# Performance work log

Measured on AMD Instinct MI355X. Metric: run time of the kernel, lower is better.

Reference implementation:

```python
import jax, jax.numpy as jnp
import numpy as np

B, NBLK, D, DY, NDIM, NMC, DH = 4096, 12, 2, 2, 24, 256, 100
SQRT3 = 3.0 ** 0.5
G2 = np.array([[1.0, 0.0], [0.5, SQRT3 / 2.0]], dtype=np.float32)
G = jnp.asarray(np.kron(np.eye(NBLK, dtype=np.float32), G2))  # (24,24) block-diag hexagonal generator
LOG_VOL = (NDIM // 2) * float(np.log(SQRT3 / 2.0))  # log sqrt(det(G G^T))


def _lin(x, w, b=None):
    y = x @ w.T
    return y if b is None else y + b


def _hex_quantize(y):
    # Exact nearest-point quantizer for the product-of-A2 (hexagonal) lattice.
    p = y.reshape(y.shape[:-1] + (NDIM // 2, 2))
    off = jnp.array([0.5, SQRT3 / 2.0], dtype=y.dtype)
    def rnd(q):  # round to rectangular sublattice Z x sqrt(3)Z
        return jnp.stack([jnp.round(q[..., 0]), jnp.round(q[..., 1] / SQRT3) * SQRT3], axis=-1)
    c0 = rnd(p)
    c1 = rnd(p - off) + off
    d0 = jnp.sum((p - c0) ** 2, axis=-1)
    d1 = jnp.sum((p - c1) ** 2, axis=-1)
    return jnp.where((d0 <= d1)[..., None], c0, c1).reshape(y.shape)


def _logits_cumulative(v, Hs, bs, fs):
    # compressai-style per-channel monotone cumulative network. v: (..., C) -> (..., C)
    v = v[..., None]  # (..., C, 1)
    for k in range(len(Hs)):
        v = jnp.einsum('coi,...ci->...co', jax.nn.softplus(Hs[k]), v) + bs[k][:, :, 0]
        if k < len(fs):
            v = v + jnp.tanh(fs[k][:, :, 0]) * jnp.tanh(v)
    return v[..., 0]


def setup_inputs() -> dict:
    key = jax.random.key(0)
    ks = iter(jax.random.split(key, 64))
    def nrm(shape, s=1.0):
        return jax.random.normal(next(ks), shape, jnp.float32) * s
    inp = {}
    inp['x'] = nrm((B, NBLK, D))
    inp['y_mean'] = nrm((NBLK, DY))
    inp['u'] = jax.random.uniform(next(ks), (NMC, NDIM), jnp.float32)
    inp['ga_w0'] = nrm((DH, D), D ** -0.5); inp['ga_b0'] = jnp.zeros((DH,), jnp.float32)
    inp['ga_w1'] = nrm((DH, DH), DH ** -0.5); inp['ga_b1'] = jnp.zeros((DH,), jnp.float32)
    inp['ga_w2'] = nrm((DY, DH), DH ** -0.5); inp['ga_b2'] = jnp.zeros((DY,), jnp.float32)
    inp['gs_w0'] = nrm((DH, DY), DY ** -0.5); inp['gs_b0'] = jnp.zeros((DH,), jnp.float32)
    inp['gs_w1'] = nrm((DH, DH), DH ** -0.5); inp['gs_b1'] = jnp.zeros((DH,), jnp.float32)
    inp['gs_w2'] = nrm((D, DH), DH ** -0.5); inp['gs_b2'] = jnp.zeros((D,), jnp.float32)
    inp['gac_w0'] = nrm((DH, NDIM), NDIM ** -0.5)
    inp['gac_w1'] = nrm((DH, DH), DH ** -0.5)
    inp['gac_w2'] = nrm((NDIM, DH), DH ** -0.5)
    inp['gsc_w0'] = nrm((DH, NDIM), NDIM ** -0.5)
    inp['gsc_w1'] = nrm((DH, DH), DH ** -0.5)
    inp['gsc_w2'] = nrm((NDIM, DH), DH ** -0.5)
    # factorized-prior cumulative params, layer dims 1->3->3->3->3->1
    inp['eb_H0'] = nrm((NDIM, 3, 1), 0.5)
    inp['eb_H1'] = nrm((NDIM, 3, 3), 0.5)
    inp['eb_H2'] = nrm((NDIM, 3, 3), 0.5)
    inp['eb_H3'] = nrm((NDIM, 3, 3), 0.5)
    inp['eb_H4'] = nrm((NDIM, 1, 3), 0.5)
    inp['eb_b0'] = nrm((NDIM, 3, 1), 0.5)
    inp['eb_b1'] = nrm((NDIM, 3, 1), 0.5)
    inp['eb_b2'] = nrm((NDIM, 3, 1), 0.5)
    inp['eb_b3'] = nrm((NDIM, 3, 1), 0.5)
    inp['eb_b4'] = nrm((NDIM, 1, 1), 0.5)
    inp['eb_a0'] = nrm((NDIM, 3, 1), 0.5)
    inp['eb_a1'] = nrm((NDIM, 3, 1), 0.5)
    inp['eb_a2'] = nrm((NDIM, 3, 1), 0.5)
    inp['eb_a3'] = nrm((NDIM, 3, 1), 0.5)
    return inp


def reference(x, y_mean, u, ga_w0, ga_b0, ga_w1, ga_b1, ga_w2, ga_b2,
              gs_w0, gs_b0, gs_w1, gs_b1, gs_w2, gs_b2,
              gac_w0, gac_w1, gac_w2, gsc_w0, gsc_w1, gsc_w2,
              eb_H0, eb_H1, eb_H2, eb_H3, eb_H4,
              eb_b0, eb_b1, eb_b2, eb_b3, eb_b4,
              eb_a0, eb_a1, eb_a2, eb_a3):
    lrelu, sp = jax.nn.leaky_relu, jax.nn.softplus
    # analysis transform g_a: (B, 12, 2) -> (B, 12, dy)
    y1 = _lin(lrelu(_lin(lrelu(_lin(x, ga_w0, ga_b0)), ga_w1, ga_b1)), ga_w2, ga_b2)
    # EMA zero-mean update (buffer assignment => no gradient through the mean)
    ym = jax.lax.stop_gradient(0.05 * y_mean + 0.95 * jnp.mean(y1, axis=0))
    y1 = (y1 - ym).reshape(B, NDIM)
    # coupled analysis transform g_a_c (Softplus MLP, no bias)
    y1 = _lin(sp(_lin(sp(_lin(y1, gac_w0)), gac_w1)), gac_w2)
    # quasi-uniform samples from the Voronoi cell of the lattice origin
    u2 = u @ G
    u2 = u2 - _hex_quantize(u2)
    # lattice quantization with straight-through estimator
    y_q = _hex_quantize(y1)
    y_hat = y1 + jax.lax.stop_gradient(y_q - y1)
    # Monte-Carlo log-likelihood over the Voronoi cell with factorized prior density
    Hs = (eb_H0, eb_H1, eb_H2, eb_H3, eb_H4)
    bs = (eb_b0, eb_b1, eb_b2, eb_b3, eb_b4)
    fs = (eb_a0, eb_a1, eb_a2, eb_a3)
    pts = y_hat[:, None, :] + u2[None, :, :]  # (B, NMC, NDIM)
    def cdf(p):
        return jax.nn.sigmoid(_logits_cumulative(p, Hs, bs, fs))
    _, pdf = jax.jvp(cdf, (pts,), (jnp.ones_like(pts),))  # density = d/dx cdf(x)
    logp = jnp.sum(jnp.log(pdf + 1e-9), axis=-1)  # (B, NMC)
    lik = jax.scipy.special.logsumexp(logp, axis=1) - jnp.log(jnp.float32(NMC)) + LOG_VOL  # (B,)
    # synthesis transforms
    y_hat1 = _lin(sp(_lin(sp(_lin(y_hat, gsc_w0)), gsc_w1)), gsc_w2).reshape(B, NBLK, DY) + ym
    x_hat = _lin(lrelu(_lin(lrelu(_lin(y_hat1, gs_w0, gs_b0)), gs_w1, gs_b1)), gs_w2, gs_b2)
    return (x_hat, lik)
```

## Files before the change

### kernel.cpp

```cpp
#include <hip/hip_runtime.h>
#include <hip/hip_bf16.h>
#include <math.h>
#include <limits.h>

constexpr int NB    = 4096;
constexpr int ROWS2 = NB * 12;
constexpr int GA_BLOCKS = ROWS2 / 128;
constexpr int GS_BLOCKS = ROWS2 / 64;
constexpr int TBL_CAP = 64;
constexpr int KBASE   = -32;

constexpr size_t WS_Y1    = 0;
constexpr size_t WS_YHAT  = 98304;
constexpr size_t WS_YHAT1 = 196608;
constexpr size_t WS_YM    = 294912;
constexpr size_t WS_U2T   = 294936;
constexpr size_t WS_EB    = 301080;
constexpr size_t WS_PART  = 302472;
constexpr size_t WS_W1T   = 320904;
constexpr size_t WS_W1BF  = 359304;
constexpr size_t WS_TBL   = 366472;
constexpr size_t WS_END   = WS_TBL + 24 * TBL_CAP * 256;

constexpr float STEP_ODD = 0.8660254037844386f;
constexpr float INV_ODD  = 1.1547005383792517f;

typedef __attribute__((ext_vector_type(8))) short bf16x8;
typedef __attribute__((ext_vector_type(4))) float f32x4;

__device__ __forceinline__ float lrelu(float x) { return x >= 0.f ? x : 0.01f * x; }
__device__ __forceinline__ float rcp_fast(float x) { return __builtin_amdgcn_rcpf(x); }

__device__ __forceinline__ unsigned short f2bf(float f) {
    unsigned b = __float_as_uint(f);
    b += 0x7FFFu + ((b >> 16) & 1u);
    return (unsigned short)(b >> 16);
}

__device__ __forceinline__ float tanh_fast(float x) {
    float xx = fminf(fmaxf(x, -15.f), 15.f);
    float e = __expf(xx + xx);
    return fmaf(-2.f, rcp_fast(e + 1.f), 1.f);
}
__device__ __forceinline__ float splus(float x) {
    return fmaxf(x, 0.f) + __logf(1.f + __expf(-fabsf(x)));
}
__device__ __forceinline__ float splus_precise(float x) {
    return fmaxf(x, 0.f) + log1pf(expf(-fabsf(x)));
}

__device__ __forceinline__ void fma4(float4& a, float h, const float4& w) {
    a.x = fmaf(h, w.x, a.x); a.y = fmaf(h, w.y, a.y);
    a.z = fmaf(h, w.z, a.z); a.w = fmaf(h, w.w, a.w);
}

__device__ __forceinline__ void hexq(float p0, float p1, float& q0, float& q1) {
    const float S3 = 1.7320508075688772f;
    const float H3 = 0.8660254037844386f;
    float c00 = rintf(p0);
    float c01 = rintf(p1 / S3) * S3;
    float c10 = rintf(p0 - 0.5f) + 0.5f;
    float c11 = rintf((p1 - H3) / S3) * S3 + H3;
    float d0 = (p0 - c00) * (p0 - c00) + (p1 - c01) * (p1 - c01);
    float d1 = (p0 - c10) * (p0 - c10) + (p1 - c11) * (p1 - c11);
    bool take0 = d0 <= d1;
    q0 = take0 ? c00 : c10;
    q1 = take0 ? c01 : c11;
}

__device__ __forceinline__ float logpdf_ch(const float* __restrict__ P, float p) {
    float w00 = P[0], w01 = P[1], w02 = P[2];
    float z0 = fmaf(w00, p, P[3]);
    float z1 = fmaf(w01, p, P[4]);
    float z2 = fmaf(w02, p, P[5]);
    float a0 = P[6], a1 = P[7], a2 = P[8];
    float e0 = tanh_fast(z0), e1 = tanh_fast(z1), e2 = tanh_fast(z2);
    float h0 = fmaf(a0, e0, z0), h1 = fmaf(a1, e1, z1), h2 = fmaf(a2, e2, z2);
    float t0 = w00 * fmaf(a0, fmaf(-e0, e0, 1.f), 1.f);
    float t1 = w01 * fmaf(a1, fmaf(-e1, e1, 1.f), 1.f);
    float t2 = w02 * fmaf(a2, fmaf(-e2, e2, 1.f), 1.f);

#define EB_LAYER(O)                                                            \
    {                                                                          \
        float z0n = fmaf(P[O+0], h0, fmaf(P[O+1], h1, fmaf(P[O+2], h2, P[O+9])));  \
        float z1n = fmaf(P[O+3], h0, fmaf(P[O+4], h1, fmaf(P[O+5], h2, P[O+10]))); \
        float z2n = fmaf(P[O+6], h0, fmaf(P[O+7], h1, fmaf(P[O+8], h2, P[O+11]))); \
        float s0 = fmaf(P[O+0], t0, fmaf(P[O+1], t1, P[O+2] * t2));            \
        float s1 = fmaf(P[O+3], t0, fmaf(P[O+4], t1, P[O+5] * t2));            \
        float s2 = fmaf(P[O+6], t0, fmaf(P[O+7], t1, P[O+8] * t2));            \
        float g0 = P[O+12], g1 = P[O+13], g2 = P[O+14];                        \
        float q0 = tanh_fast(z0n), q1 = tanh_fast(z1n), q2 = tanh_fast(z2n);   \
        h0 = fmaf(g0, q0, z0n); h1 = fmaf(g1, q1, z1n); h2 = fmaf(g2, q2, z2n); \
        t0 = s0 * fmaf(g0, fmaf(-q0, q0, 1.f), 1.f);                           \
        t1 = s1 * fmaf(g1, fmaf(-q1, q1, 1.f), 1.f);                           \
        t2 = s2 * fmaf(g2, fmaf(-q2, q2, 1.f), 1.f);                           \
    }
    EB_LAYER(9)
    EB_LAYER(24)
    EB_LAYER(39)
#undef EB_LAYER

    float L = fmaf(P[54], h0, fmaf(P[55], h1, fmaf(P[56], h2, P[57])));
    float T = fmaf(P[54], t0, fmaf(P[55], t1, P[56] * t2));
    float Lc = fminf(fmaxf(L, -30.f), 30.f);
    float sg = rcp_fast(1.f + __expf(-Lc));
    float pdf = sg * (1.f - sg) * T;
    return __logf(pdf + 1e-9f);
}

__global__ __launch_bounds__(256) void k_prep(
    const float* __restrict__ H0p, const float* __restrict__ H1p,
    const float* __restrict__ H2p, const float* __restrict__ H3p,
    const float* __restrict__ H4p,
    const float* __restrict__ b0p, const float* __restrict__ b1p,
    const float* __restrict__ b2p, const float* __restrict__ b3p,
    const float* __restrict__ b4p,
    const float* __restrict__ a0p, const float* __restrict__ a1p,
    const float* __restrict__ a2p, const float* __restrict__ a3p,
    const float* __restrict__ u,
    const float* __restrict__ w1ga, const float* __restrict__ w1gac,
    const float* __restrict__ w1gsc, const float* __restrict__ w1gs,
    float* __restrict__ eb, float* __restrict__ u2t,
    float* __restrict__ w1t, float* __restrict__ w1bf)
{
    int tid = threadIdx.x;
    if (blockIdx.x > 0) {
        int t = blockIdx.x - 1;
        if (t < 150) {
            int m = t / 50;
            int o = (t % 50) * 256 + tid;
            int k = o >> 7, i = o & 127;
            const float* src = (m == 0) ? w1ga : (m == 1) ? w1gac : w1gsc;
            w1t[m * 12800 + o] = (i < 100) ? src[i * 100 + k] : 0.f;
        } else {
            int o = (t - 150) * 256 + tid;
            int i = o >> 7, k = o & 127;
            float v = (i < 100 && k < 100) ? w1gs[i * 100 + k] : 0.f;
            ((unsigned short*)w1bf)[o] = f2bf(v);
        }
        return;
    }
    if (tid < 24) {
        int c = tid;
        float* P = eb + c * 58;
        for (int j = 0; j < 3; ++j) P[j]      = splus_precise(H0p[c*3+j]);
        for (int j = 0; j < 3; ++j) P[3+j]    = b0p[c*3+j];
        for (int j = 0; j < 3; ++j) P[6+j]    = tanhf(a0p[c*3+j]);
        for (int j = 0; j < 9; ++j) P[9+j]    = splus_precise(H1p[c*9+j]);
        for (int j = 0; j < 3; ++j) P[18+j]   = b1p[c*3+j];
        for (int j = 0; j < 3; ++j) P[21+j]   = tanhf(a1p[c*3+j]);
        for (int j = 0; j < 9; ++j) P[24+j]   = splus_precise(H2p[c*9+j]);
        for (int j = 0; j < 3; ++j) P[33+j]   = b2p[c*3+j];
        for (int j = 0; j < 3; ++j) P[36+j]   = tanhf(a2p[c*3+j]);
        for (int j = 0; j < 9; ++j) P[39+j]   = splus_precise(H3p[c*9+j]);
        for (int j = 0; j < 3; ++j) P[48+j]   = b3p[c*3+j];
        for (int j = 0; j < 3; ++j) P[51+j]   = tanhf(a3p[c*3+j]);
        for (int j = 0; j < 3; ++j) P[54+j]   = splus_precise(H4p[c*3+j]);
        P[57] = b4p[c];
    }
    int m = tid;
    if (m < 256) {
        for (int j = 0; j < 12; ++j) {
            float a  = u[m*24 + 2*j];
            float bb = u[m*24 + 2*j + 1];
            float p0 = fmaf(0.5f, bb, a);
            float p1 = 0.8660254037844386f * bb;
            float q0, q1; hexq(p0, p1, q0, q1);
            u2t[(2*j)   * 256 + m] = p0 - q0;
            u2t[(2*j+1) * 256 + m] = p1 - q1;
        }
    }
}

template <int MEAN>
__device__ __forceinline__ void gemm2_body(
    int bid,
    const float* __restrict__ in,
    const float* __restrict__ w0, const float* __restrict__ b0,
    const float* __restrict__ w1t,
    const float* __restrict__ b1, const float* __restrict__ w2,
    const float* __restrict__ b2,
    float* __restrict__ out, float* __restrict__ partial)
{
    __shared__ alignas(16) float shT[100 * 128];
    __shared__ float S[128][2];

    int tid = threadIdx.x;
    int row0 = bid * 128;

    for (int e = tid; e < 12800; e += 256) {
        int j = e >> 7, row = e & 127;
        float2 xv = ((const float2*)in)[row0 + row];
        shT[j * 128 + row] =
            lrelu(fmaf(w0[2*j], xv.x, fmaf(w0[2*j+1], xv.y, b0[j])));
    }

    int rg = tid >> 4;
    int cg = tid & 15;
    __syncthreads();

    float4 acc0[8], acc1[8];
    float4 zero4 = make_float4(0.f, 0.f, 0.f, 0.f);
#pragma unroll
    for (int r = 0; r < 8; ++r) { acc0[r] = zero4; acc1[r] = zero4; }

    const float4* wg = (const float4*)w1t + cg * 2;
    const float4* hp = (const float4*)shT + rg * 2;
    float4 wa0 = wg[0],  wa1 = wg[1];
    float4 wb0 = wg[32], wb1 = wg[33];
#pragma unroll 2
    for (int k = 0; k < 100; ++k) {
        float4 wn0 = wg[(k + 2) * 32];
        float4 wn1 = wg[(k + 2) * 32 + 1];
        float4 ha = hp[k * 32];
        float4 hb = hp[k * 32 + 1];
        fma4(acc0[0], ha.x, wa0); fma4(acc1[0], ha.x, wa1);
        fma4(acc0[1], ha.y, wa0); fma4(acc1[1], ha.y, wa1);
        fma4(acc0[2], ha.z, wa0); fma4(acc1[2], ha.z, wa1);
        fma4(acc0[3], ha.w, wa0); fma4(acc1[3], ha.w, wa1);
        fma4(acc0[4], hb.x, wa0); fma4(acc1[4], hb.x, wa1);
        fma4(acc0[5], hb.y, wa0); fma4(acc1[5], hb.y, wa1);
        fma4(acc0[6], hb.z, wa0); fma4(acc1[6], hb.z, wa1);
        fma4(acc0[7], hb.w, wa0); fma4(acc1[7], hb.w, wa1);
        wa0 = wb0; wa1 = wb1; wb0 = wn0; wb1 = wn1;
    }
    __syncthreads();

    float b1v[8], w20v[8], w21v[8];
    int c0 = cg * 8;
#pragma unroll
    for (int e = 0; e < 8; ++e) {
        int c = c0 + e;
        bool v = (c < 100);
        b1v[e]  = v ? b1[c] : 0.f;
        w20v[e] = v ? w2[c] : 0.f;
        w21v[e] = v ? w2[100 + c] : 0.f;
    }
    float* red = shT;
#pragma unroll
    for (int r = 0; r < 8; ++r) {
        float a0 = lrelu(acc0[r].x + b1v[0]);
        float a1 = lrelu(acc0[r].y + b1v[1]);
        float a2 = lrelu(acc0[r].z + b1v[2]);
        float a3 = lrelu(acc0[r].w + b1v[3]);
        float a4 = lrelu(acc1[r].x + b1v[4]);
        float a5 = lrelu(acc1[r].y + b1v[5]);
        float a6 = lrelu(acc1[r].z + b1v[6]);
        float a7 = lrelu(acc1[r].w + b1v[7]);
        float y0 = a0*w20v[0] + a1*w20v[1] + a2*w20v[2] + a3*w20v[3]
                 + a4*w20v[4] + a5*w20v[5] + a6*w20v[6] + a7*w20v[7];
        float y1 = a0*w21v[0] + a1*w21v[1] + a2*w21v[2] + a3*w21v[3]
                 + a4*w21v[4] + a5*w21v[5] + a6*w21v[6] + a7*w21v[7];
        int row = rg * 8 + r;
        red[(row * 2) * 16 + cg]     = y0;
        red[(row * 2 + 1) * 16 + cg] = y1;
    }
    __syncthreads();
    {
        int row = tid >> 1, p = tid & 1;
        const float4* rp = (const float4*)&red[(row * 2 + p) * 16];
        float4 v0 = rp[0], v1 = rp[1], v2 = rp[2], v3 = rp[3];
        float s = ((v0.x + v0.y) + (v0.z + v0.w))
                + ((v1.x + v1.y) + (v1.z + v1.w))
                + ((v2.x + v2.y) + (v2.z + v2.w))
                + ((v3.x + v3.y) + (v3.z + v3.w));
        float y = s + b2[p];
        out[(row0 + row) * 2 + p] = y;
        if (MEAN) S[row][p] = y;
    }
    if (MEAN) {
        __syncthreads();
        if (tid < 24) {
            int j = tid >> 1, par = tid & 1;
            int base = row0 % 12;
            int k0 = (j - base + 144) % 12;
            float s = 0.f;
            for (int k = k0; k < 128; k += 12) s += S[k][par];
            partial[bid * 24 + tid] = s;
        }
    }
}

__device__ __forceinline__ void gs_mfma_body(
    int bid,
    const float* __restrict__ in,
    const float* __restrict__ w0, const float* __restrict__ b0,
    const float* __restrict__ w1bf,
    const float* __restrict__ b1, const float* __restrict__ w2,
    const float* __restrict__ b2,
    float* __restrict__ out)
{
    int tid = threadIdx.x;
    int lane = tid & 63, wv = tid >> 6;
    int rsel = lane & 15;
    int kgrp = lane >> 4;
    int row0w = bid * 64 + wv * 16;

    float2 xv = ((const float2*)in)[row0w + rsel];

    bf16x8 afr[4];
#pragma unroll
    for (int kb = 0; kb < 4; ++kb) {
#pragma unroll
        for (int j8 = 0; j8 < 8; ++j8) {
            int j = kb * 32 + kgrp * 8 + j8;
            float h = 0.f;
            if (j < 100)
                h = lrelu(fmaf(w0[2*j], xv.x, fmaf(w0[2*j+1], xv.y, b0[j])));
            afr[kb][j8] = (short)f2bf(h);
        }
    }

    const unsigned short* w1u = (const unsigned short*)w1bf;
    f32x4 acc[7];
#pragma unroll
    for (int n = 0; n < 7; ++n) acc[n] = (f32x4){0.f, 0.f, 0.f, 0.f};
#pragma unroll
    for (int kb = 0; kb < 4; ++kb) {
#pragma unroll
        for (int n = 0; n < 7; ++n) {
            bf16x8 bfr = *(const bf16x8*)(w1u + (n * 16 + rsel) * 128
                                              + kb * 32 + kgrp * 8);
            acc[n] = __builtin_amdgcn_mfma_f32_16x16x32_bf16(afr[kb], bfr,
                                                             acc[n], 0, 0, 0);
        }
    }

    float py0[4] = {0.f, 0.f, 0.f, 0.f}, py1[4] = {0.f, 0.f, 0.f, 0.f};
#pragma unroll
    for (int n = 0; n < 7; ++n) {
        int i = n * 16 + rsel;
        bool v = (i < 100);
        float b1v = v ? b1[i] : 0.f;
        float w20 = v ? w2[i] : 0.f;
        float w21 = v ? w2[100 + i] : 0.f;
#pragma unroll
        for (int r = 0; r < 4; ++r) {
            float a = lrelu(acc[n][r] + b1v);
            py0[r] = fmaf(a, w20, py0[r]);
            py1[r] = fmaf(a, w21, py1[r]);
        }
    }
#pragma unroll
    for (int r = 0; r < 4; ++r) {
#pragma unroll
        for (int off = 1; off < 16; off <<= 1) {
            py0[r] += __shfl_xor(py0[r], off);
            py1[r] += __shfl_xor(py1[r], off);
        }
    }
    if (rsel == 0) {
#pragma unroll
        for (int r = 0; r < 4; ++r) {
            int row = row0w + kgrp * 4 + r;
            out[row * 2]     = py0[r] + b2[0];
            out[row * 2 + 1] = py1[r] + b2[1];
        }
    }
}

__global__ __launch_bounds__(256, 2) void k_ga_table(
    const float* __restrict__ in,
    const float* __restrict__ w0, const float* __restrict__ b0,
    const float* __restrict__ w1t,
    const float* __restrict__ b1, const float* __restrict__ w2,
    const float* __restrict__ b2,
    float* __restrict__ out, float* __restrict__ partial,
    const float* __restrict__ eb, const float* __restrict__ u2t,
    float* __restrict__ tbl)
{
    if (blockIdx.x < (unsigned)GA_BLOCKS) {
        gemm2_body<1>(blockIdx.x, in, w0, b0, w1t, b1, w2, b2, out, partial);
    } else {
        int cv4 = blockIdx.x - GA_BLOCKS;
        int c = cv4 >> 4, vg = (cv4 & 15) * 4;
        int m = threadIdx.x;
        float step = (c & 1) ? STEP_ODD : 0.5f;
        float uv = u2t[c * 256 + m];
        const float* P = eb + c * 58;
#pragma unroll
        for (int dv = 0; dv < 4; ++dv) {
            int v = vg + dv;
            float val = (float)(KBASE + v) * step;
            tbl[(c * TBL_CAP + v) * 256 + m] = logpdf_ch(P, val + uv);
        }
    }
}

__global__ __launch_bounds__(256) void k_mean_final(
    const float* __restrict__ partial, const float* __restrict__ y_mean,
    float* __restrict__ ym)
{
    int tid = threadIdx.x;
    int c = tid >> 3, s = tid & 7;
    float v = 0.f;
    if (c < 24)
        for (int g = s; g < GA_BLOCKS; g += 8) v += partial[g * 24 + c];
    v += __shfl_xor(v, 1); v += __shfl_xor(v, 2); v += __shfl_xor(v, 4);
    if (c < 24 && s == 0)
        ym[c] = fmaf(0.05f, y_mean[c], 0.95f * (v * (1.0f / NB)));
}

__global__ __launch_bounds__(256, 4) void k_fused24(
    const float* __restrict__ y1,
    const float* __restrict__ w0A, const float* __restrict__ w1tA,
    const float* __restrict__ w2A,
    const float* __restrict__ w0B, const float* __restrict__ w1tB,
    const float* __restrict__ w2B,
    const float* __restrict__ ymg,
    float* __restrict__ yhat, float* __restrict__ yhat1)
{
    __shared__ float sw0[2400];
    __shared__ float sw2[2400];
    __shared__ float sX[8 * 25];
    __shared__ float sO[8 * 25];
    __shared__ alignas(16) float h0[100 * 8];
    __shared__ float h1[100 * 8];
    __shared__ float symL[24];

    int tid = threadIdx.x;
    int row0 = blockIdx.x * 8;

    if (tid < 24) symL[tid] = ymg[tid];
    __syncthreads();
    for (int e = tid; e < 192; e += 256) {
        int r = e / 24, c = e - r * 24;
        sX[r * 25 + c] = y1[row0 * 24 + e] - symL[c];
    }

    int ii = tid & 127, rg = tid >> 7;

    for (int pass = 0; pass < 2; ++pass) {
        const float* w0  = pass ? w0B  : w0A;
        const float* w1t = pass ? w1tB : w1tA;
        const float* w2  = pass ? w2B  : w2A;
        for (int t = tid; t < 2400; t += 256) {
            sw0[t] = w0[t];
            sw2[t] = w2[t];
        }
        __syncthreads();

        for (int e = tid; e < 800; e += 256) {
            int j = e >> 3, r = e & 7;
            const float* wr = sw0 + j * 24;
            const float* xr = sX + r * 25;
            float a = 0.f, b = 0.f;
#pragma unroll
            for (int k = 0; k < 24; k += 2) {
                a = fmaf(wr[k],     xr[k],     a);
                b = fmaf(wr[k + 1], xr[k + 1], b);
            }
            h0[j * 8 + r] = splus(a + b);
        }
        __syncthreads();

        {
            float4 a = make_float4(0.f, 0.f, 0.f, 0.f);
            const float* wc = w1t + ii;
            const float4* h4 = (const float4*)h0 + rg;
#pragma unroll 4
            for (int j = 0; j < 100; ++j) {
                float w = wc[j * 128];
                float4 h = h4[j * 2];
                a.x = fmaf(w, h.x, a.x); a.y = fmaf(w, h.y, a.y);
                a.z = fmaf(w, h.z, a.z); a.w = fmaf(w, h.w, a.w);
            }
            if (ii < 100) {
                h1[ii * 8 + rg * 4]     = splus(a.x);
                h1[ii * 8 + rg * 4 + 1] = splus(a.y);
                h1[ii * 8 + rg * 4 + 2] = splus(a.z);
                h1[ii * 8 + rg * 4 + 3] = splus(a.w);
            }
        }
        __syncthreads();

        if (tid < 192) {
            int c = tid >> 3, r = tid & 7;
            const float* w2r = sw2 + c * 100;
            float s = 0.f, s2 = 0.f;
#pragma unroll 4
            for (int i = 0; i < 100; i += 2) {
                s  = fmaf(w2r[i],     h1[i * 8 + r],       s);
                s2 = fmaf(w2r[i + 1], h1[(i + 1) * 8 + r], s2);
            }
            float v = s + s2;
            if (pass == 0) sO[r * 25 + c] = v;
            else yhat1[(row0 + r) * 24 + c] = v + symL[c];
        }

        if (pass == 0) {
            __syncthreads();
            if (tid < 96) {
                int pr = tid >> 3, r = tid & 7;
                float v0 = sO[r * 25 + 2*pr], v1 = sO[r * 25 + 2*pr + 1];
                float q0, q1; hexq(v0, v1, q0, q1);
                yhat[(row0 + r) * 24 + 2*pr]     = q0;
                yhat[(row0 + r) * 24 + 2*pr + 1] = q1;
                sX[r * 25 + 2*pr]     = q0;
                sX[r * 25 + 2*pr + 1] = q1;
            }
        }
    }
}

__global__ __launch_bounds__(256, 4) void k_gs_mc(
    const float* __restrict__ yhat1,
    const float* __restrict__ w0, const float* __restrict__ b0,
    const float* __restrict__ w1bf,
    const float* __restrict__ b1, const float* __restrict__ w2,
    const float* __restrict__ b2, float* __restrict__ xhat,
    const float* __restrict__ yhat, const float* __restrict__ u2t,
    const float* __restrict__ eb,
    const float* __restrict__ tbl, float* __restrict__ lik)
{
    if (blockIdx.x < (unsigned)GS_BLOCKS) {
        gs_mfma_body(blockIdx.x, yhat1, w0, b0, w1bf, b1, w2, b2, xhat);
        return;
    }
    __shared__ float sy[4 * 24];
    __shared__ float redm[4], reds[4];
    int tid = threadIdx.x;
    int wv = tid >> 6;
    int bg = (blockIdx.x - GS_BLOCKS) * 4;

    if (tid < 96) sy[tid] = yhat[bg * 24 + tid];
    __syncthreads();

    for (int q = 0; q < 4; ++q) {
        float lp = 0.f;
        unsigned miss = 0;
#pragma unroll
        for (int c = 0; c < 24; ++c) {
            float yv = sy[q * 24 + c];
            float inv = (c & 1) ? INV_ODD : 2.0f;
            int k = (int)rintf(yv * inv);
            int idx = k - KBASE;
            bool ok = (idx >= 0 && idx < TBL_CAP);
            int idq = min(max(idx, 0), TBL_CAP - 1);
            float tv = tbl[(c * TBL_CAP + idq) * 256 + tid];
            lp += ok ? tv : 0.f;
            if (!ok) miss |= (1u << c);
        }
        while (miss) {
            int c = __ffs(miss) - 1;
            miss &= miss - 1;
            lp += logpdf_ch(eb + c * 58, sy[q * 24 + c] + u2t[c * 256 + tid]);
        }

        float m = lp;
#pragma unroll
        for (int off = 1; off < 64; off <<= 1) m = fmaxf(m, __shfl_xor(m, off));
        if ((tid & 63) == 0) redm[wv] = m;
        __syncthreads();
        float mx = fmaxf(fmaxf(redm[0], redm[1]), fmaxf(redm[2], redm[3]));
        float e = __expf(lp - mx);
#pragma unroll
        for (int off = 1; off < 64; off <<= 1) e += __shfl_xor(e, off);
        if ((tid & 63) == 0) reds[wv] = e;
        __syncthreads();
        if (tid == 0)
            lik[bg + q] = mx + __logf(reds[0] + reds[1] + reds[2] + reds[3])
                        - 7.271269879190247f;
        __syncthreads();
    }
}

__global__ __launch_bounds__(256, 4) void k_gs(
    const float* __restrict__ yhat1,
    const float* __restrict__ w0, const float* __restrict__ b0,
    const float* __restrict__ w1bf,
    const float* __restrict__ b1, const float* __restrict__ w2,
    const float* __restrict__ b2, float* __restrict__ xhat)
{
    gs_mfma_body(blockIdx.x, yhat1, w0, b0, w1bf, b1, w2, b2, xhat);
}

__global__ __launch_bounds__(256) void k_mc_direct(
    const float* __restrict__ yhat, const float* __restrict__ u2t,
    const float* __restrict__ eb, float* __restrict__ lik)
{
    __shared__ alignas(16) float sU[24 * 256];
    __shared__ float redm[4], reds[4];
    int tid = threadIdx.x;
    int wv = tid >> 6;
    int b = blockIdx.x;
    for (int i = tid; i < 1536; i += 256)
        ((float4*)sU)[i] = ((const float4*)u2t)[i];
    __syncthreads();

    float lp = 0.f;
    for (int c = 0; c < 24; ++c)
        lp += logpdf_ch(eb + c * 58, yhat[b * 24 + c] + sU[c * 256 + tid]);

    float m = lp;
#pragma unroll
    for (int off = 1; off < 64; off <<= 1) m = fmaxf(m, __shfl_xor(m, off));
    if ((tid & 63) == 0) redm[wv] = m;
    __syncthreads();
    float mx = fmaxf(fmaxf(redm[0], redm[1]), fmaxf(redm[2], redm[3]));
    float e = __expf(lp - mx);
#pragma unroll
    for (int off = 1; off < 64; off <<= 1) e += __shfl_xor(e, off);
    if ((tid & 63) == 0) reds[wv] = e;
    __syncthreads();
    if (tid == 0)
        lik[b] = mx + __logf(reds[0] + reds[1] + reds[2] + reds[3])
               - 7.271269879190247f;
}

extern "C" void kernel_launch(void* const* d_in, const int* in_sizes, int n_in,
                              void* d_out, int out_size, void* d_ws, size_t ws_size,
                              hipStream_t stream)
{
    (void)in_sizes; (void)n_in; (void)out_size;
    const float* x      = (const float*)d_in[0];
    const float* y_mean = (const float*)d_in[1];
    const float* u      = (const float*)d_in[2];
    const float* ga_w0  = (const float*)d_in[3];
    const float* ga_b0  = (const float*)d_in[4];
    const float* ga_w1  = (const float*)d_in[5];
    const float* ga_b1  = (const float*)d_in[6];
    const float* ga_w2  = (const float*)d_in[7];
    const float* ga_b2  = (const float*)d_in[8];
    const float* gs_w0  = (const float*)d_in[9];
    const float* gs_b0  = (const float*)d_in[10];
    const float* gs_w1  = (const float*)d_in[11];
    const float* gs_b1  = (const float*)d_in[12];
    const float* gs_w2  = (const float*)d_in[13];
    const float* gs_b2  = (const float*)d_in[14];
    const float* gac_w0 = (const float*)d_in[15];
    const float* gac_w1 = (const float*)d_in[16];
    const float* gac_w2 = (const float*)d_in[17];
    const float* gsc_w0 = (const float*)d_in[18];
    const float* gsc_w1 = (const float*)d_in[19];
    const float* gsc_w2 = (const float*)d_in[20];
    const float* eb_H0  = (const float*)d_in[21];
    const float* eb_H1  = (const float*)d_in[22];
    const float* eb_H2  = (const float*)d_in[23];
    const float* eb_H3  = (const float*)d_in[24];
    const float* eb_H4  = (const float*)d_in[25];
    const float* eb_b0  = (const float*)d_in[26];
    const float* eb_b1  = (const float*)d_in[27];
    const float* eb_b2  = (const float*)d_in[28];
    const float* eb_b3  = (const float*)d_in[29];
    const float* eb_b4  = (const float*)d_in[30];
    const float* eb_a0  = (const float*)d_in[31];
    const float* eb_a1  = (const float*)d_in[32];
    const float* eb_a2  = (const float*)d_in[33];
    const float* eb_a3  = (const float*)d_in[34];

    float* ws    = (float*)d_ws;
    float* y1    = ws + WS_Y1;
    float* yhat  = ws + WS_YHAT;
    float* yhat1 = ws + WS_YHAT1;
    float* ym    = ws + WS_YM;
    float* u2t   = ws + WS_U2T;
    float* eb    = ws + WS_EB;
    float* part  = ws + WS_PART;
    float* w1t   = ws + WS_W1T;
    float* w1bf  = ws + WS_W1BF;
    float* tbl   = ws + WS_TBL;
    float* xhat  = (float*)d_out;
    float* lik   = (float*)d_out + 98304;

    float* w1tGA  = w1t;
    float* w1tGAC = w1t + 12800;
    float* w1tGSC = w1t + 25600;

    bool use_tbl = ws_size >= WS_END * sizeof(float);

    k_prep<<<207, 256, 0, stream>>>(eb_H0, eb_H1, eb_H2, eb_H3, eb_H4,
                                    eb_b0, eb_b1, eb_b2, eb_b3, eb_b4,
                                    eb_a0, eb_a1, eb_a2, eb_a3, u,
                                    ga_w1, gac_w1, gsc_w1, gs_w1,
                                    eb, u2t, w1t, w1bf);
    if (use_tbl)
        k_ga_table<<<GA_BLOCKS + 24 * TBL_CAP / 4, 256, 0, stream>>>(
            x, ga_w0, ga_b0, w1tGA, ga_b1, ga_w2, ga_b2, y1, part,
            eb, u2t, tbl);
    else
        k_ga_table<<<GA_BLOCKS, 256, 0, stream>>>(
            x, ga_w0, ga_b0, w1tGA, ga_b1, ga_w2, ga_b2, y1, part,
            eb, u2t, tbl);
    k_mean_final<<<1, 256, 0, stream>>>(part, y_mean, ym);
    k_fused24<<<NB / 8, 256, 0, stream>>>(y1, gac_w0, w1tGAC, gac_w2,
                                          gsc_w0, w1tGSC, gsc_w2,
                                          ym, yhat, yhat1);
    if (use_tbl) {
        k_gs_mc<<<GS_BLOCKS + NB / 4, 256, 0, stream>>>(
            yhat1, gs_w0, gs_b0, w1bf, gs_b1, gs_w2, gs_b2, xhat,
            yhat, u2t, eb, tbl, lik);
    } else {
        k_gs<<<GS_BLOCKS, 256, 0, stream>>>(
            yhat1, gs_w0, gs_b0, w1bf, gs_b1, gs_w2, gs_b2, xhat);
        k_mc_direct<<<NB, 256, 0, stream>>>(yhat, u2t, eb, lik);
    }
}
```

Measured before the change: 113.6 us.

## Move gsc synthesis MLP to bf16 MFMA and co-schedule it with MC likelihood

The fused 24-dim kernel is split. The gac analysis pass stays in scalar FP32, and the gsc synthesis MLP (24→100→100→24) gets a new bf16 MFMA body, with its weights pre-converted to bf16 in the prep kernel. The gsc blocks now share a launch with the Monte-Carlo likelihood blocks, and the gs MLP runs as a separate kernel afterward. This adds one kernel launch, puts the gsc path in bf16, and adds a block-wide sync inside the MFMA body.

New measurement: 167.1 us. 47.1% more time.

```diff
diff --git a/kernel.cpp b/kernel.cpp
--- a/kernel.cpp
+++ b/kernel.cpp
@@ -7,6 +7,7 @@
 constexpr int ROWS2 = NB * 12;
 constexpr int GA_BLOCKS = ROWS2 / 128;
 constexpr int GS_BLOCKS = ROWS2 / 64;
+constexpr int GSC_BLOCKS = NB / 64;
 constexpr int TBL_CAP = 64;
 constexpr int KBASE   = -32;
 
@@ -18,8 +19,10 @@
 constexpr size_t WS_EB    = 301080;
 constexpr size_t WS_PART  = 302472;
 constexpr size_t WS_W1T   = 320904;
-constexpr size_t WS_W1BF  = 359304;
-constexpr size_t WS_TBL   = 366472;
+constexpr size_t WS_W1BFGS  = 346504;
+constexpr size_t WS_W1BFGSC = 350088;
+constexpr size_t WS_W2BFGSC = 358280;
+constexpr size_t WS_TBL   = 360328;
 constexpr size_t WS_END   = WS_TBL + 24 * TBL_CAP * 256;
 
 constexpr float STEP_ODD = 0.8660254037844386f;
@@ -119,24 +122,36 @@
     const float* __restrict__ a2p, const float* __restrict__ a3p,
     const float* __restrict__ u,
     const float* __restrict__ w1ga, const float* __restrict__ w1gac,
-    const float* __restrict__ w1gsc, const float* __restrict__ w1gs,
+    const float* __restrict__ w1gs, const float* __restrict__ w1gsc,
+    const float* __restrict__ w2gsc,
     float* __restrict__ eb, float* __restrict__ u2t,
-    float* __restrict__ w1t, float* __restrict__ w1bf)
+    float* __restrict__ w1t, float* __restrict__ w1bfGS,
+    float* __restrict__ w1bfGSC, float* __restrict__ w2bfGSC)
 {
     int tid = threadIdx.x;
     if (blockIdx.x > 0) {
         int t = blockIdx.x - 1;
-        if (t < 150) {
+        if (t < 100) {
             int m = t / 50;
             int o = (t % 50) * 256 + tid;
             int k = o >> 7, i = o & 127;
-            const float* src = (m == 0) ? w1ga : (m == 1) ? w1gac : w1gsc;
+            const float* src = (m == 0) ? w1ga : w1gac;
             w1t[m * 12800 + o] = (i < 100) ? src[i * 100 + k] : 0.f;
-        } else {
-            int o = (t - 150) * 256 + tid;
+        } else if (t < 156) {
+            int o = (t - 100) * 256 + tid;
             int i = o >> 7, k = o & 127;
             float v = (i < 100 && k < 100) ? w1gs[i * 100 + k] : 0.f;
-            ((unsigned short*)w1bf)[o] = f2bf(v);
+            ((unsigned short*)w1bfGS)[o] = f2bf(v);
+        } else if (t < 220) {
+            int o = (t - 156) * 256 + tid;
+            int i = o >> 7, k = o & 127;
+            float v = (i < 100 && k < 100) ? w1gsc[i * 100 + k] : 0.f;
+            ((unsigned short*)w1bfGSC)[o] = f2bf(v);
+        } else {
+            int o = (t - 220) * 256 + tid;
+            int c = o >> 7, k = o & 127;
+            float v = (c < 24 && k < 100) ? w2gsc[c * 100 + k] : 0.f;
+            ((unsigned short*)w2bfGSC)[o] = f2bf(v);
         }
         return;
     }
@@ -359,6 +374,115 @@
     }
 }
 
+__device__ __forceinline__ void gsc_mfma_body(
+    int bid,
+    const float* __restrict__ yhat,
+    const float* __restrict__ w0,
+    const float* __restrict__ w1bfC, const float* __restrict__ w2bfC,
+    const float* __restrict__ ymg, float* __restrict__ yhat1,
+    float* __restrict__ h1L )
+{
+    int tid = threadIdx.x;
+    int lane = tid & 63, wv = tid >> 6;
+    int rsel = lane & 15;
+    int kgrp = lane >> 4;
+    int row0w = bid * 64 + wv * 16;
+
+    float xr[24];
+    const float4* xp = (const float4*)(yhat + (row0w + rsel) * 24);
+#pragma unroll
+    for (int k4 = 0; k4 < 6; ++k4) {
+        float4 t = xp[k4];
+        xr[4*k4] = t.x; xr[4*k4+1] = t.y; xr[4*k4+2] = t.z; xr[4*k4+3] = t.w;
+    }
+
+    bf16x8 afr[4];
+#pragma unroll
+    for (int kb = 0; kb < 4; ++kb) {
+#pragma unroll
+        for (int j8 = 0; j8 < 8; ++j8) {
+            int j = kb * 32 + kgrp * 8 + j8;
+            float h = 0.f;
+            if (j < 100) {
+                const float* wr = w0 + j * 24;
+                float a = 0.f, b = 0.f;
+#pragma unroll
+                for (int k = 0; k < 24; k += 2) {
+                    a = fmaf(wr[k],     xr[k],     a);
+                    b = fmaf(wr[k + 1], xr[k + 1], b);
+                }
+                h = splus(a + b);
+            }
+            afr[kb][j8] = (short)f2bf(h);
+        }
+    }
+
+    const unsigned short* w1u = (const unsigned short*)w1bfC;
+    f32x4 acc[8];
+#pragma unroll
+    for (int n = 0; n < 8; ++n) acc[n] = (f32x4){0.f, 0.f, 0.f, 0.f};
+#pragma unroll
+    for (int kb = 0; kb < 4; ++kb) {
+#pragma unroll
+        for (int n = 0; n < 8; ++n) {
+            bf16x8 bfr = *(const bf16x8*)(w1u + (n * 16 + rsel) * 128
+                                              + kb * 32 + kgrp * 8);
+            acc[n] = __builtin_amdgcn_mfma_f32_16x16x32_bf16(afr[kb], bfr,
+                                                             acc[n], 0, 0, 0);
+        }
+    }
+
+    float* hl = h1L + wv * 128 * 16;
+#pragma unroll
+    for (int n = 0; n < 8; ++n) {
+        int i = n * 16 + rsel;
+        float v0 = (i < 100) ? splus(acc[n][0]) : 0.f;
+        float v1 = (i < 100) ? splus(acc[n][1]) : 0.f;
+        float v2 = (i < 100) ? splus(acc[n][2]) : 0.f;
+        float v3 = (i < 100) ? splus(acc[n][3]) : 0.f;
+        hl[i * 16 + kgrp * 4]     = v0;
+        hl[i * 16 + kgrp * 4 + 1] = v1;
+        hl[i * 16 + kgrp * 4 + 2] = v2;
+        hl[i * 16 + kgrp * 4 + 3] = v3;
+    }
+    __syncthreads();
+
+    bf16x8 afr2[4];
+#pragma unroll
+    for (int kb = 0; kb < 4; ++kb) {
+#pragma unroll
+        for (int j8 = 0; j8 < 8; ++j8) {
+            int i = kb * 32 + kgrp * 8 + j8;
+            afr2[kb][j8] = (short)f2bf(hl[i * 16 + rsel]);
+        }
+    }
+    const unsigned short* w2u = (const unsigned short*)w2bfC;
+    f32x4 acc2[2];
+    acc2[0] = (f32x4){0.f, 0.f, 0.f, 0.f};
+    acc2[1] = (f32x4){0.f, 0.f, 0.f, 0.f};
+#pragma unroll
+    for (int kb = 0; kb < 4; ++kb) {
+#pragma unroll
+        for (int n = 0; n < 2; ++n) {
+            bf16x8 bfr = *(const bf16x8*)(w2u + (n * 16 + rsel) * 128
+                                              + kb * 32 + kgrp * 8);
+            acc2[n] = __builtin_amdgcn_mfma_f32_16x16x32_bf16(afr2[kb], bfr,
+                                                              acc2[n], 0, 0, 0);
+        }
+    }
+
+#pragma unroll
+    for (int n = 0; n < 2; ++n) {
+        int c = n * 16 + rsel;
+        if (c < 24) {
+            float ym = ymg[c];
+#pragma unroll
+            for (int r = 0; r < 4; ++r)
+                yhat1[(row0w + kgrp * 4 + r) * 24 + c] = acc2[n][r] + ym;
+        }
+    }
+}
+
 __global__ __launch_bounds__(256, 2) void k_ga_table(
     const float* __restrict__ in,
     const float* __restrict__ w0, const float* __restrict__ b0,
@@ -401,14 +525,12 @@
         ym[c] = fmaf(0.05f, y_mean[c], 0.95f * (v * (1.0f / NB)));
 }
 
-__global__ __launch_bounds__(256, 4) void k_fused24(
+__global__ __launch_bounds__(256, 4) void k_gac(
     const float* __restrict__ y1,
     const float* __restrict__ w0A, const float* __restrict__ w1tA,
     const float* __restrict__ w2A,
-    const float* __restrict__ w0B, const float* __restrict__ w1tB,
-    const float* __restrict__ w2B,
     const float* __restrict__ ymg,
-    float* __restrict__ yhat, float* __restrict__ yhat1)
+    float* __restrict__ yhat)
 {
     __shared__ float sw0[2400];
     __shared__ float sw2[2400];
@@ -422,106 +544,92 @@
     int row0 = blockIdx.x * 8;
 
     if (tid < 24) symL[tid] = ymg[tid];
+    for (int t = tid; t < 2400; t += 256) {
+        sw0[t] = w0A[t];
+        sw2[t] = w2A[t];
+    }
     __syncthreads();
     for (int e = tid; e < 192; e += 256) {
         int r = e / 24, c = e - r * 24;
         sX[r * 25 + c] = y1[row0 * 24 + e] - symL[c];
     }
+    __syncthreads();
 
     int ii = tid & 127, rg = tid >> 7;
 
-    for (int pass = 0; pass < 2; ++pass) {
-        const float* w0  = pass ? w0B  : w0A;
-        const float* w1t = pass ? w1tB : w1tA;
-        const float* w2  = pass ? w2B  : w2A;
-        for (int t = tid; t < 2400; t += 256) {
-            sw0[t] = w0[t];
-            sw2[t] = w2[t];
-        }
-        __syncthreads();
-
-        for (int e = tid; e < 800; e += 256) {
-            int j = e >> 3, r = e & 7;
-            const float* wr = sw0 + j * 24;
-            const float* xr = sX + r * 25;
-            float a = 0.f, b = 0.f;
-#pragma unroll
-            for (int k = 0; k < 24; k += 2) {
-                a = fmaf(wr[k],     xr[k],     a);
-                b = fmaf(wr[k + 1], xr[k + 1], b);
-            }
-            h0[j * 8 + r] = splus(a + b);
-        }
-        __syncthreads();
-
-        {
-            float4 a = make_float4(0.f, 0.f, 0.f, 0.f);
-            const float* wc = w1t + ii;
-            const float4* h4 = (const float4*)h0 + rg;
+    for (int e = tid; e < 800; e += 256) {
+        int j = e >> 3, r = e & 7;
+        const float* wr = sw0 + j * 24;
+        const float* xr = sX + r * 25;
+        float a = 0.f, b = 0.f;
+#pragma unroll
+        for (int k = 0; k < 24; k += 2) {
+            a = fmaf(wr[k],     xr[k],     a);
+            b = fmaf(wr[k + 1], xr[k + 1], b);
+        }
+        h0[j * 8 + r] = splus(a + b);
+    }
+    __syncthreads();
+
+    {
+        float4 a = make_float4(0.f, 0.f, 0.f, 0.f);
+        const float* wc = w1tA + ii;
+        const float4* h4 = (const float4*)h0 + rg;
 #pragma unroll 4
-            for (int j = 0; j < 100; ++j) {
-                float w = wc[j * 128];
-                float4 h = h4[j * 2];
-                a.x = fmaf(w, h.x, a.x); a.y = fmaf(w, h.y, a.y);
-                a.z = fmaf(w, h.z, a.z); a.w = fmaf(w, h.w, a.w);
-            }
-            if (ii < 100) {
-                h1[ii * 8 + rg * 4]     = splus(a.x);
-                h1[ii * 8 + rg * 4 + 1] = splus(a.y);
-                h1[ii * 8 + rg * 4 + 2] = splus(a.z);
-                h1[ii * 8 + rg * 4 + 3] = splus(a.w);
-            }
-        }
-        __syncthreads();
-
-        if (tid < 192) {
-            int c = tid >> 3, r = tid & 7;
-            const float* w2r = sw2 + c * 100;
-            float s = 0.f, s2 = 0.f;
+        for (int j = 0; j < 100; ++j) {
+            float w = wc[j * 128];
+            float4 h = h4[j * 2];
+            a.x = fmaf(w, h.x, a.x); a.y = fmaf(w, h.y, a.y);
+            a.z = fmaf(w, h.z, a.z); a.w = fmaf(w, h.w, a.w);
+        }
+        if (ii < 100) {
+            h1[ii * 8 + rg * 4]     = splus(a.x);
+            h1[ii * 8 + rg * 4 + 1] = splus(a.y);
+            h1[ii * 8 + rg * 4 + 2] = splus(a.z);
+            h1[ii * 8 + rg * 4 + 3] = splus(a.w);
+        }
+    }
+    __syncthreads();
+
+    if (tid < 192) {
+        int c = tid >> 3, r = tid & 7;
+        const float* w2r = sw2 + c * 100;
+        float s = 0.f, s2 = 0.f;
 #pragma unroll 4
-            for (int i = 0; i < 100; i += 2) {
-                s  = fmaf(w2r[i],     h1[i * 8 + r],       s);
-                s2 = fmaf(w2r[i + 1], h1[(i + 1) * 8 + r], s2);
-            }
-            float v = s + s2;
-            if (pass == 0) sO[r * 25 + c] = v;
-            else yhat1[(row0 + r) * 24 + c] = v + symL[c];
-        }
-
-        if (pass == 0) {
-            __syncthreads();
-            if (tid < 96) {
-                int pr = tid >> 3, r = tid & 7;
-                float v0 = sO[r * 25 + 2*pr], v1 = sO[r * 25 + 2*pr + 1];
-                float q0, q1; hexq(v0, v1, q0, q1);
-                yhat[(row0 + r) * 24 + 2*pr]     = q0;
-                yhat[(row0 + r) * 24 + 2*pr + 1] = q1;
-                sX[r * 25 + 2*pr]     = q0;
-                sX[r * 25 + 2*pr + 1] = q1;
-            }
-        }
-    }
-}
-
-__global__ __launch_bounds__(256, 4) void k_gs_mc(
-    const float* __restrict__ yhat1,
-    const float* __restrict__ w0, const float* __restrict__ b0,
-    const float* __restrict__ w1bf,
-    const float* __restrict__ b1, const float* __restrict__ w2,
-    const float* __restrict__ b2, float* __restrict__ xhat,
-    const float* __restrict__ yhat, const float* __restrict__ u2t,
-    const float* __restrict__ eb,
+        for (int i = 0; i < 100; i += 2) {
+            s  = fmaf(w2r[i],     h1[i * 8 + r],       s);
+            s2 = fmaf(w2r[i + 1], h1[(i + 1) * 8 + r], s2);
+        }
+        sO[r * 25 + c] = s + s2;
+    }
+    __syncthreads();
+    if (tid < 96) {
+        int pr = tid >> 3, r = tid & 7;
+        float v0 = sO[r * 25 + 2*pr], v1 = sO[r * 25 + 2*pr + 1];
+        float q0, q1; hexq(v0, v1, q0, q1);
+        yhat[(row0 + r) * 24 + 2*pr]     = q0;
+        yhat[(row0 + r) * 24 + 2*pr + 1] = q1;
+    }
+}
+
+__global__ __launch_bounds__(256, 4) void k_gsc_mc(
+    const float* __restrict__ yhat,
+    const float* __restrict__ w0C, const float* __restrict__ w1bfC,
+    const float* __restrict__ w2bfC, const float* __restrict__ ymg,
+    float* __restrict__ yhat1,
+    const float* __restrict__ u2t, const float* __restrict__ eb,
     const float* __restrict__ tbl, float* __restrict__ lik)
 {
-    if (blockIdx.x < (unsigned)GS_BLOCKS) {
-        gs_mfma_body(blockIdx.x, yhat1, w0, b0, w1bf, b1, w2, b2, xhat);
+    __shared__ float h1L[4 * 128 * 16];
+    if (blockIdx.x < (unsigned)GSC_BLOCKS) {
+        gsc_mfma_body(blockIdx.x, yhat, w0C, w1bfC, w2bfC, ymg, yhat1, h1L);
         return;
     }
-    __shared__ float sy[4 * 24];
+    float* sy = h1L;
     __shared__ float redm[4], reds[4];
     int tid = threadIdx.x;
     int wv = tid >> 6;
-    int bg = (blockIdx.x - GS_BLOCKS) * 4;
+    int bg = (blockIdx.x - GSC_BLOCKS) * 4;
 
     if (tid < 96) sy[tid] = yhat[bg * 24 + tid];
     __syncthreads();
@@ -658,22 +766,23 @@
     float* eb    = ws + WS_EB;
     float* part  = ws + WS_PART;
     float* w1t   = ws + WS_W1T;
-    float* w1bf  = ws + WS_W1BF;
+    float* w1bfGS  = ws + WS_W1BFGS;
+    float* w1bfGSC = ws + WS_W1BFGSC;
+    float* w2bfGSC = ws + WS_W2BFGSC;
     float* tbl   = ws + WS_TBL;
     float* xhat  = (float*)d_out;
     float* lik   = (float*)d_out + 98304;
 
     float* w1tGA  = w1t;
     float* w1tGAC = w1t + 12800;
-    float* w1tGSC = w1t + 25600;
 
     bool use_tbl = ws_size >= WS_END * sizeof(float);
 
-    k_prep<<<207, 256, 0, stream>>>(eb_H0, eb_H1, eb_H2, eb_H3, eb_H4,
+    k_prep<<<237, 256, 0, stream>>>(eb_H0, eb_H1, eb_H2, eb_H3, eb_H4,
                                     eb_b0, eb_b1, eb_b2, eb_b3, eb_b4,
                                     eb_a0, eb_a1, eb_a2, eb_a3, u,
-                                    ga_w1, gac_w1, gsc_w1, gs_w1,
-                                    eb, u2t, w1t, w1bf);
+                                    ga_w1, gac_w1, gs_w1, gsc_w1, gsc_w2,
+                                    eb, u2t, w1t, w1bfGS, w1bfGSC, w2bfGSC);
     if (use_tbl)
         k_ga_table<<<GA_BLOCKS + 24 * TBL_CAP / 4, 256, 0, stream>>>(
             x, ga_w0, ga_b0, w1tGA, ga_b1, ga_w2, ga_b2, y1, part,
@@ -683,16 +792,17 @@
             x, ga_w0, ga_b0, w1tGA, ga_b1, ga_w2, ga_b2, y1, part,
             eb, u2t, tbl);
     k_mean_final<<<1, 256, 0, stream>>>(part, y_mean, ym);
-    k_fused24<<<NB / 8, 256, 0, stream>>>(y1, gac_w0, w1tGAC, gac_w2,
-                                          gsc_w0, w1tGSC, gsc_w2,
-                                          ym, yhat, yhat1);
+    k_gac<<<NB / 8, 256, 0, stream>>>(y1, gac_w0, w1tGAC, gac_w2, ym, yhat);
     if (use_tbl) {
-        k_gs_mc<<<GS_BLOCKS + NB / 4, 256, 0, stream>>>(
-            yhat1, gs_w0, gs_b0, w1bf, gs_b1, gs_w2, gs_b2, xhat,
-            yhat, u2t, eb, tbl, lik);
+        k_gsc_mc<<<GSC_BLOCKS + NB / 4, 256, 0, stream>>>(
+            yhat, gsc_w0, w1bfGSC, w2bfGSC, ym, yhat1,
+            u2t, eb, tbl, lik);
     } else {
-        k_gs<<<GS_BLOCKS, 256, 0, stream>>>(
-            yhat1, gs_w0, gs_b0, w1bf, gs_b1, gs_w2, gs_b2, xhat);
+        k_gsc_mc<<<GSC_BLOCKS, 256, 0, stream>>>(
+            yhat, gsc_w0, w1bfGSC, w2bfGSC, ym, yhat1,
+            u2t, eb, tbl, lik);
         k_mc_direct<<<NB, 256, 0, stream>>>(yhat, u2t, eb, lik);
     }
-}
+    k_gs<<<GS_BLOCKS, 256, 0, stream>>>(yhat1, gs_w0, gs_b0, w1bfGS,
+                                        gs_b1, gs_w2, gs_b2, xhat);
+}
```
